# Kernel optimization log

Measured on AMD Instinct MI355X. Metric: run time of the kernel, lower is better.

The kernel has to match this reference:

```python
import jax, jax.numpy as jnp
import numpy as np

B, N = 16, 16384
K = 16        # num_keypoints
LATENT = 128
CAGE = 8
BN_EPS = 1e-5


def setup_inputs():
    key = jax.random.key(0)
    ks = jax.random.split(key, 40)
    def rn(i, shape, s=1.0):
        return jax.random.normal(ks[i], shape, dtype=jnp.float32) * s
    inp = {
        "source_points": rn(0, (B, N, 3)),
        "target_points": rn(1, (B, N, 3)),
        "enc_w1": rn(2, (64, 3), 0.3), "enc_b1": rn(3, (64,), 0.1),
        "bn1_gamma": 1.0 + rn(4, (64,), 0.1), "bn1_beta": rn(5, (64,), 0.1),
        "bn1_mean": rn(6, (64,), 0.1), "bn1_var": 0.5 + jax.random.uniform(ks[7], (64,), dtype=jnp.float32),
        "enc_w2": rn(8, (128, 64), 0.1), "enc_b2": rn(9, (128,), 0.1),
        "bn2_gamma": 1.0 + rn(10, (128,), 0.1), "bn2_beta": rn(11, (128,), 0.1),
        "bn2_mean": rn(12, (128,), 0.1), "bn2_var": 0.5 + jax.random.uniform(ks[13], (128,), dtype=jnp.float32),
        "enc_w3": rn(14, (LATENT, 128), 0.1), "enc_b3": rn(15, (LATENT,), 0.1),
        "bn3_gamma": 1.0 + rn(16, (LATENT,), 0.1), "bn3_beta": rn(17, (LATENT,), 0.1),
        "bn3_mean": rn(18, (LATENT,), 0.1), "bn3_var": 0.5 + jax.random.uniform(ks[19], (LATENT,), dtype=jnp.float32),
        "kp_w1": rn(20, (128, LATENT), 0.1), "kp_b1": rn(21, (128,), 0.1),
        "kp_w2": rn(22, (K * 3, 128), 0.1), "kp_b2": rn(23, (K * 3,), 0.1),
        "cg_w1": rn(24, (128, K * 3), 0.1), "cg_b1": rn(25, (128,), 0.1),
        "cg_w2": rn(26, (CAGE ** 3 * 3, 128), 0.05), "cg_b2": rn(27, (CAGE ** 3 * 3,), 0.01),
    }
    return inp


def _bn(x, g, b, m, v):
    # inference-mode BatchNorm1d over channel (last) dim
    return (x - m) * jax.lax.rsqrt(v + BN_EPS) * g + b


def _encode(pts, w1, b1, g1, be1, m1, v1, w2, b2, g2, be2, m2, v2, w3, b3, g3, be3, m3, v3):
    # pointwise 1x1 convs == per-point linear layers; pts: (B, N, 3)
    h = jax.nn.relu(_bn(jnp.einsum('bnc,oc->bno', pts, w1) + b1, g1, be1, m1, v1))
    h = jax.nn.relu(_bn(jnp.einsum('bnc,oc->bno', h, w2) + b2, g2, be2, m2, v2))
    h = jax.nn.relu(_bn(jnp.einsum('bnc,oc->bno', h, w3) + b3, g3, be3, m3, v3))
    return h.max(axis=1)  # global max-pool -> (B, LATENT)


def _fps_one(pts, kps):
    # pts: (N,3), kps: (K,3). Same math as the torch loop: iterative farthest-point
    # selection; recomputing cdist to selected[:i] each step == incremental min-dist.
    # squared distances preserve argmax/min of euclidean distances.
    d0 = jnp.sum((pts[:, None, :] - kps[None, :, :]) ** 2, -1).min(axis=1)
    sel0 = pts[jnp.argmax(d0)]
    mind = jnp.sum((pts - sel0) ** 2, -1)
    def step(mind, _):
        sel = pts[jnp.argmax(mind)]
        return jnp.minimum(mind, jnp.sum((pts - sel) ** 2, -1)), sel
    _, sels = jax.lax.scan(step, mind, None, length=K - 1)
    return jnp.concatenate([sel0[None], sels], axis=0)  # (K, 3)


def _fps(points, keypoints):
    return jax.vmap(_fps_one)(points, keypoints)


def _cage_deform(pts, disp):
    # pts: (B,N,3), disp: (B,C,C,C,3). Batched trilinear interpolation on the cage.
    C = CAGE
    lin = jnp.linspace(0.0, 1.0, C)
    grid = jnp.stack(jnp.meshgrid(lin, lin, lin, indexing='ij'), axis=-1)
    cage = grid[None] + disp
    cf = cage.reshape(cage.shape[0], C * C * C, 3)
    pmin = pts.min(axis=1, keepdims=True)
    pmax = pts.max(axis=1, keepdims=True)
    t = (pts - pmin) / (pmax - pmin + 1e-6) * (C - 1)
    idx = jnp.clip(t.astype(jnp.int32), 0, C - 2)   # trunc == floor (t >= 0)
    w = t - idx.astype(t.dtype)
    u, v, z = idx[..., 0], idx[..., 1], idx[..., 2]
    wx, wy, wz = w[..., 0:1], w[..., 1:2], w[..., 2:3]
    def corner(du, dv, dz):
        flat = (u + du) * C * C + (v + dv) * C + (z + dz)      # (B,N)
        flat = jnp.broadcast_to(flat[..., None], flat.shape + (3,))
        return jnp.take_along_axis(cf, flat, axis=1)            # (B,N,3)
    d = ((1 - wx) * (1 - wy) * (1 - wz) * corner(0, 0, 0)
         + wx * (1 - wy) * (1 - wz) * corner(1, 0, 0)
         + (1 - wx) * wy * (1 - wz) * corner(0, 1, 0)
         + wx * wy * (1 - wz) * corner(1, 1, 0)
         + (1 - wx) * (1 - wy) * wz * corner(0, 0, 1)
         + wx * (1 - wy) * wz * corner(1, 0, 1)
         + (1 - wx) * wy * wz * corner(0, 1, 1)
         + wx * wy * wz * corner(1, 1, 1))
    return pts + d


def reference(source_points, target_points, enc_w1, enc_b1, bn1_gamma, bn1_beta, bn1_mean, bn1_var, enc_w2, enc_b2, bn2_gamma, bn2_beta, bn2_mean, bn2_var, enc_w3, enc_b3, bn3_gamma, bn3_beta, bn3_mean, bn3_var, kp_w1, kp_b1, kp_w2, kp_b2, cg_w1, cg_b1, cg_w2, cg_b2):
    enc = lambda p: _encode(p, enc_w1, enc_b1, bn1_gamma, bn1_beta, bn1_mean, bn1_var,
                            enc_w2, enc_b2, bn2_gamma, bn2_beta, bn2_mean, bn2_var,
                            enc_w3, enc_b3, bn3_gamma, bn3_beta, bn3_mean, bn3_var)
    src_lat = enc(source_points)
    tgt_lat = enc(target_points)
    kp = lambda lat: (jax.nn.relu(lat @ kp_w1.T + kp_b1) @ kp_w2.T + kp_b2).reshape(-1, K, 3)
    src_kp = _fps(source_points, kp(src_lat))
    tgt_kp = _fps(target_points, kp(tgt_lat))
    diff = (tgt_kp - src_kp).reshape(-1, K * 3)
    disp = (jax.nn.relu(diff @ cg_w1.T + cg_b1) @ cg_w2.T + cg_b2).reshape(-1, CAGE, CAGE, CAGE, 3)
    deformed = _cage_deform(source_points, disp)
    return (deformed, src_kp, tgt_kp)
```

## Files before the change

kernel.cpp:

```cpp
#include <hip/hip_runtime.h>

#define B_ 16
#define N_ 16384
#define K_ 16

enum : int {
  WS_LAT  = 0,
  WS_SEL  = 5632,
  WS_PMIN = 7168,
  WS_PMAX = 7216,
  WS_CF   = 7264,
  WS_W1F  = 31840,
  WS_B1F  = 32032,
  WS_WB2H = 32096,
  WS_WB2L = 36192,
  WS_B2F  = 40288,
  WS_WB3H = 40416,
  WS_B3F  = 56800,
  WS_WB3L = 56928,
  WS_END  = 73312
};

enum : int { OUT_DEF=0, OUT_SRCKP=786432, OUT_TGTKP=787200 };

typedef _Float16 f16x8 __attribute__((ext_vector_type(8)));
typedef _Float16 f16x2 __attribute__((ext_vector_type(2)));
typedef float    f32x16 __attribute__((ext_vector_type(16)));

__device__ __forceinline__ float dist2rn(float px,float py,float pz,float sx,float sy,float sz){
  float dx=__fsub_rn(px,sx), dy=__fsub_rn(py,sy), dz=__fsub_rn(pz,sz);
  return __fadd_rn(__fadd_rn(__fmul_rn(dx,dx),__fmul_rn(dy,dy)),__fmul_rn(dz,dz));
}

struct EncW {
  const float *w1,*b1,*g1,*be1,*m1,*v1;
  const float *w2,*b2,*g2,*be2,*m2,*v2;
  const float *w3,*b3,*g3,*be3,*m3,*v3;
};

__device__ __forceinline__ float bn_scale(const float* g, const float* v, int ch){
  return g[ch] * (1.0f / sqrtf(v[ch] + 1e-5f));
}

__global__ void prep_kernel(EncW a, float* ws){
  const int stride = gridDim.x*blockDim.x;
  const int tid = blockIdx.x*blockDim.x + threadIdx.x;
  for (int i=tid;i<4096;i+=stride)
    ws[WS_LAT+i] = 0.0f;
  for (int i=tid;i<192;i+=stride){
    int o=i/3;
    ws[WS_W1F+i] = a.w1[i] * bn_scale(a.g1,a.v1,o);
  }
  for (int i=tid;i<64;i+=stride){
    float s = bn_scale(a.g1,a.v1,i);
    ws[WS_B1F+i] = (a.b1[i] - a.m1[i])*s + a.be1[i];
  }
  for (int i=tid;i<8192;i+=stride){
    int j = i & 7, frag = i >> 3;
    int l = frag & 63, wk = frag >> 6;
    int kt = wk & 3, wn = wk >> 2;
    int c = kt*16 + ((l>>5)<<3) + j;
    int o = wn*32 + (l&31);
    float v = a.w2[o*64+c] * bn_scale(a.g2,a.v2,o);
    _Float16 h = (_Float16)v;
    ((_Float16*)(ws+WS_WB2H))[i] = h;
    ((_Float16*)(ws+WS_WB2L))[i] = (_Float16)(v - (float)h);
  }
  for (int i=tid;i<128;i+=stride){
    float s = bn_scale(a.g2,a.v2,i);
    ws[WS_B2F+i] = (a.b2[i] - a.m2[i])*s + a.be2[i];
  }
  for (int i=tid;i<16384;i+=stride){
    int j = i & 7, frag = i >> 3;
    int l = frag & 63, wk = frag >> 6;
    int kt = wk & 7, wn = wk >> 3;
    int c = kt*16 + ((l>>5)<<3) + j;
    int o = wn*32 + (l&31);
    float v = a.w3[o*128+c] * bn_scale(a.g3,a.v3,o);
    _Float16 h = (_Float16)v;
    ((_Float16*)(ws+WS_WB3H))[i] = h;
    ((_Float16*)(ws+WS_WB3L))[i] = (_Float16)(v - (float)h);
  }
  for (int i=tid;i<128;i+=stride){
    float s = bn_scale(a.g3,a.v3,i);
    ws[WS_B3F+i] = (a.b3[i] - a.m3[i])*s + a.be3[i];
  }
}

__global__ __launch_bounds__(256, 5) void encode_kernel(const float* __restrict__ src,
                                                        const float* __restrict__ tgt,
                                                        const float* __restrict__ ws,
                                                        float* __restrict__ lat){
  const int cloud = blockIdx.y;
  const int tile  = blockIdx.x;
  const int t = threadIdx.x;
  const int lane = t & 63;
  const int wn = __builtin_amdgcn_readfirstlane(t >> 6);
  const int l31 = lane & 31;
  const int hb  = lane >> 5;
  const int swz = (l31 & 7) << 3;

  __shared__ alignas(16) _Float16 A[16384];

  const float* base = ((cloud < B_) ? (src + (size_t)cloud*N_*3)
                                    : (tgt + (size_t)(cloud-B_)*N_*3))
                      + (size_t)tile*64*3;

  f16x8 b2h[4], b2l[4];
  {
    const _Float16* wb2h = (const _Float16*)(ws + WS_WB2H);
    const _Float16* wb2l = (const _Float16*)(ws + WS_WB2L);
    #pragma unroll
    for (int kt=0; kt<4; kt++){
      const int fi = ((wn*4 + kt)*64 + lane)*8;
      b2h[kt] = *(const f16x8*)(wb2h + fi);
      b2l[kt] = *(const f16x8*)(wb2l + fi);
    }
  }

  {
    const int pt = t >> 2, q = t & 3;
    const float x = base[pt*3+0], y = base[pt*3+1], z = base[pt*3+2];
    const float* w1 = ws + WS_W1F;
    const float* b1 = ws + WS_B1F;
    const int swz1 = (pt & 7) << 3;
    _Float16* AH1 = A;
    _Float16* AL1 = A + 4096;
    #pragma unroll
    for (int cc = 0; cc < 16; cc += 2){
      const int o = q*16 + cc;
      float v0 = fmaf(w1[o*3+2], z, fmaf(w1[o*3+1], y, w1[o*3+0]*x)) + b1[o];
      float v1 = fmaf(w1[o*3+5], z, fmaf(w1[o*3+4], y, w1[o*3+3]*x)) + b1[o+1];
      v0 = fmaxf(v0, 0.0f); v1 = fmaxf(v1, 0.0f);
      f16x2 h, l;
      h[0] = (_Float16)v0;              h[1] = (_Float16)v1;
      l[0] = (_Float16)(v0 - (float)h[0]); l[1] = (_Float16)(v1 - (float)h[1]);
      const int idx = (pt*64 + o) ^ swz1;
      *(f16x2*)&AH1[idx] = h;
      *(f16x2*)&AL1[idx] = l;
    }
  }

  int koff[8];
  #pragma unroll
  for (int kt=0; kt<8; kt++) koff[kt] = (((kt*16) | (hb*8)) ^ swz) << 1;

  __syncthreads();

  f32x16 acc2[2];
  #pragma unroll
  for (int e=0;e<16;e++){ acc2[0][e]=0.0f; acc2[1][e]=0.0f; }
  {
    const char* pA2 = (const char*)A + l31*128;
    #pragma unroll
    for (int kt=0; kt<4; kt++){
      #pragma unroll
      for (int m=0;m<2;m++){
        const f16x8 ah = *(const f16x8*)(pA2 + m*4096 + koff[kt]);
        const f16x8 al = *(const f16x8*)(pA2 + m*4096 + koff[kt] + 8192);
        acc2[m] = __builtin_amdgcn_mfma_f32_32x32x16_f16(ah, b2h[kt], acc2[m], 0,0,0);
        acc2[m] = __builtin_amdgcn_mfma_f32_32x32x16_f16(ah, b2l[kt], acc2[m], 0,0,0);
        acc2[m] = __builtin_amdgcn_mfma_f32_32x32x16_f16(al, b2h[kt], acc2[m], 0,0,0);
      }
    }
  }
  __syncthreads();

  const int ch = wn*32 + l31;
  {
    const float b = ws[WS_B2F + ch];
    char* pWr[4];
    #pragma unroll
    for (int r4=0;r4<4;r4++)
      pWr[r4] = (char*)A + (r4 + 4*hb)*256 + ((ch ^ ((r4 + 4*hb) << 3)) << 1);
    #pragma unroll
    for (int r4=0;r4<4;r4++){
      #pragma unroll
      for (int rq=0;rq<4;rq++){
        const int reg = rq*4 + r4;
        #pragma unroll
        for (int m=0;m<2;m++){
          const float v = fmaxf(acc2[m][reg] + b, 0.0f);
          const _Float16 hi = (_Float16)v;
          const _Float16 lo = (_Float16)(v - (float)hi);
          char* pw = pWr[r4] + rq*2048 + m*8192;
          *(_Float16*)(pw) = hi;
          *(_Float16*)(pw + 16384) = lo;
        }
      }
    }
  }
  __syncthreads();

  f32x16 acc3[2];
  #pragma unroll
  for (int e=0;e<16;e++){ acc3[0][e]=0.0f; acc3[1][e]=0.0f; }
  {
    const _Float16* wb3h = (const _Float16*)(ws + WS_WB3H);
    const _Float16* wb3l = (const _Float16*)(ws + WS_WB3L);
    const char* pA3 = (const char*)A + l31*256;
    #pragma unroll
    for (int kt=0; kt<8; kt++){
      const int fi = ((wn*8 + kt)*64 + lane)*8;
      const f16x8 bh = *(const f16x8*)(wb3h + fi);
      const f16x8 bl = *(const f16x8*)(wb3l + fi);
      #pragma unroll
      for (int m=0;m<2;m++){
        const f16x8 ah = *(const f16x8*)(pA3 + m*8192 + koff[kt]);
        const f16x8 al = *(const f16x8*)(pA3 + m*8192 + koff[kt] + 16384);
        acc3[m] = __builtin_amdgcn_mfma_f32_32x32x16_f16(ah, bh, acc3[m], 0,0,0);
        acc3[m] = __builtin_amdgcn_mfma_f32_32x32x16_f16(ah, bl, acc3[m], 0,0,0);
        acc3[m] = __builtin_amdgcn_mfma_f32_32x32x16_f16(al, bh, acc3[m], 0,0,0);
      }
    }
  }

  {
    const float b = ws[WS_B3F + ch];
    float x = 0.0f;
    #pragma unroll
    for (int m=0;m<2;m++){
      #pragma unroll
      for (int r=0;r<16;r++)
        x = fmaxf(x, acc3[m][r] + b);
    }
    x = fmaxf(x, __shfl_xor(x, 32, 64));
    if (lane < 32)
      atomicMax((unsigned*)(lat + cloud*128 + ch), __float_as_uint(x));
  }
}

__device__ __forceinline__ void fps_round(int r, int t, int wv,
                                          float bv, int bi, float bx, float by, float bz,
                                          float (*cv)[16], int (*ci)[16],
                                          float (*cx)[16], float (*cy)[16], float (*cz)[16],
                                          float* ws, float* out, int cloud,
                                          float& s0, float& s1, float& s2){
  float v = bv; int i = bi;
  #pragma unroll
  for (int m=1;m<64;m<<=1){
    float v2=__shfl_xor(v,m,64); int i2=__shfl_xor(i,m,64);
    if (v2 > v || (v2 == v && i2 < i)){ v=v2; i=i2; }
  }
  const int p = r & 1;
  if ((i >> 4) == t){ cv[p][wv]=v; ci[p][wv]=i; cx[p][wv]=bx; cy[p][wv]=by; cz[p][wv]=bz; }
  __syncthreads();
  float wvv = cv[p][0]; int wi = ci[p][0]; int slot = 0;
  #pragma unroll
  for (int e=1;e<16;e++){
    float v2=cv[p][e]; int i2=ci[p][e];
    if (v2 > wvv || (v2 == wvv && i2 < wi)){ wvv=v2; wi=i2; slot=e; }
  }
  s0 = cx[p][slot]; s1 = cy[p][slot]; s2 = cz[p][slot];
  if (t == 0){
    float* sw = ws + WS_SEL + cloud*48 + r*3;
    sw[0]=s0; sw[1]=s1; sw[2]=s2;
    size_t o = (cloud<B_) ? (size_t)(OUT_SRCKP + cloud*48 + r*3)
                          : (size_t)(OUT_TGTKP + (cloud-B_)*48 + r*3);
    out[o]=s0; out[o+1]=s1; out[o+2]=s2;
  }
}

__global__ __launch_bounds__(1024, 4) void fps_kernel(const float* __restrict__ src,
                                                      const float* __restrict__ tgt,
                                                      const float* __restrict__ kw1,
                                                      const float* __restrict__ kb1,
                                                      const float* __restrict__ kw2,
                                                      const float* __restrict__ kb2,
                                                      float* ws, float* out){
  const int cloud = blockIdx.x; const int t = threadIdx.x;
  const int wv = t >> 6;
  const int lane = t & 63;
  const float* base = (cloud < B_) ? (src + (size_t)cloud*N_*3)
                                   : (tgt + (size_t)cloud*N_*3 - (size_t)B_*N_*3);
  __shared__ alignas(16) float kpl[48];
  __shared__ alignas(16) float h[128];
  __shared__ float cv[2][16]; __shared__ int ci[2][16];
  __shared__ float cx[2][16]; __shared__ float cy[2][16]; __shared__ float cz[2][16];
  __shared__ float red[96];

  float px[16], py[16], pz[16];
  {
    float4 raw[12];
    const float4* b4 = (const float4*)(base + (size_t)t*48);
    #pragma unroll
    for (int q=0;q<12;q++) raw[q] = b4[q];
    #pragma unroll
    for (int q=0;q<4;q++){
      float4 va=raw[q*3], vb=raw[q*3+1], vc=raw[q*3+2];
      px[q*4  ]=va.x; py[q*4  ]=va.y; pz[q*4  ]=va.z;
      px[q*4+1]=va.w; py[q*4+1]=vb.x; pz[q*4+1]=vb.y;
      px[q*4+2]=vb.z; py[q*4+2]=vb.w; pz[q*4+2]=vc.x;
      px[q*4+3]=vc.y; py[q*4+3]=vc.z; pz[q*4+3]=vc.w;
    }
  }
  #pragma unroll
  for (int k=0;k<16;k++){
    asm volatile("" : "+v"(px[k]), "+v"(py[k]), "+v"(pz[k]));
  }

  const float* lat = ws + WS_LAT + cloud*128;
  if (t < 128){
    float acc = kb1[t];
    const float4* w4 = (const float4*)(kw1 + t*128);
    const float4* l4 = (const float4*)lat;
    #pragma unroll 8
    for (int c4=0;c4<32;c4++){
      float4 wq=w4[c4], lq=l4[c4];
      acc = fmaf(lq.x, wq.x, acc);
      acc = fmaf(lq.y, wq.y, acc);
      acc = fmaf(lq.z, wq.z, acc);
      acc = fmaf(lq.w, wq.w, acc);
    }
    h[t] = fmaxf(acc, 0.0f);
  }
  __syncthreads();
  if (t < 48){
    float acc = kb2[t];
    const float4* w4 = (const float4*)(kw2 + t*128);
    #pragma unroll 8
    for (int c4=0;c4<32;c4++){
      float4 wq=w4[c4];
      float4 hq=*(const float4*)&h[c4*4];
      acc = fmaf(hq.x, wq.x, acc);
      acc = fmaf(hq.y, wq.y, acc);
      acc = fmaf(hq.z, wq.z, acc);
      acc = fmaf(hq.w, wq.w, acc);
    }
    kpl[t] = acc;
  }

  if (cloud < B_){
    float mn0=3.4e38f,mn1=3.4e38f,mn2=3.4e38f, mx0=-3.4e38f,mx1=-3.4e38f,mx2=-3.4e38f;
    #pragma unroll
    for (int k=0;k<16;k++){
      mn0=fminf(mn0,px[k]); mn1=fminf(mn1,py[k]); mn2=fminf(mn2,pz[k]);
      mx0=fmaxf(mx0,px[k]); mx1=fmaxf(mx1,py[k]); mx2=fmaxf(mx2,pz[k]);
    }
    #pragma unroll
    for (int m=1;m<64;m<<=1){
      mn0=fminf(mn0,__shfl_xor(mn0,m,64)); mx0=fmaxf(mx0,__shfl_xor(mx0,m,64));
      mn1=fminf(mn1,__shfl_xor(mn1,m,64)); mx1=fmaxf(mx1,__shfl_xor(mx1,m,64));
      mn2=fminf(mn2,__shfl_xor(mn2,m,64)); mx2=fmaxf(mx2,__shfl_xor(mx2,m,64));
    }
    if (lane==0){
      red[wv*6+0]=mn0; red[wv*6+1]=mn1; red[wv*6+2]=mn2;
      red[wv*6+3]=mx0; red[wv*6+4]=mx1; red[wv*6+5]=mx2;
    }
    __syncthreads();
    if (t < 6){
      float v = red[t];
      for (int e=1;e<16;e++){
        float v2 = red[e*6+t];
        v = (t<3) ? fminf(v,v2) : fmaxf(v,v2);
      }
      if (t<3) ws[WS_PMIN + cloud*3 + t] = v;
      else     ws[WS_PMAX + cloud*3 + (t-3)] = v;
    }
  }
  __syncthreads();

  float mind[16];
  #pragma unroll
  for (int k=0;k<16;k++) mind[k] = 3.4028235e38f;
  for (int j=0;j<K_;j++){
    const float sx=kpl[j*3], sy=kpl[j*3+1], sz=kpl[j*3+2];
    #pragma unroll
    for (int k=0;k<16;k++)
      mind[k] = fminf(mind[k], dist2rn(px[k],py[k],pz[k], sx,sy,sz));
  }

  float bv = -1.0f; int bi = 0; float bx=0.f, by=0.f, bz=0.f;
  #pragma unroll
  for (int k=0;k<16;k++){
    if (mind[k] > bv){ bv=mind[k]; bi=t*16+k; bx=px[k]; by=py[k]; bz=pz[k]; }
  }
  float s0, s1, s2;
  fps_round(0, t, wv, bv, bi, bx, by, bz, cv, ci, cx, cy, cz, ws, out, cloud, s0, s1, s2);

  bv = -1.0f; bi = 0;
  #pragma unroll
  for (int k=0;k<16;k++){
    float d = dist2rn(px[k],py[k],pz[k], s0,s1,s2);
    mind[k] = d;
    if (d > bv){ bv=d; bi=t*16+k; bx=px[k]; by=py[k]; bz=pz[k]; }
  }
  fps_round(1, t, wv, bv, bi, bx, by, bz, cv, ci, cx, cy, cz, ws, out, cloud, s0, s1, s2);

  for (int r=2; r<K_; ++r){
    bv = -1.0f; bi = 0;
    #pragma unroll
    for (int k=0;k<16;k++){
      float d = dist2rn(px[k],py[k],pz[k], s0,s1,s2);
      float m = fminf(mind[k], d);
      mind[k] = m;
      if (m > bv){ bv=m; bi=t*16+k; bx=px[k]; by=py[k]; bz=pz[k]; }
    }
    fps_round(r, t, wv, bv, bi, bx, by, bz, cv, ci, cx, cy, cz, ws, out, cloud, s0, s1, s2);
  }
}

__global__ __launch_bounds__(256) void deform_kernel(const float* __restrict__ src,
                                                     const float* __restrict__ cw1,
                                                     const float* __restrict__ cb1,
                                                     const float* __restrict__ cw2,
                                                     const float* __restrict__ cb2,
                                                     const float* __restrict__ ws,
                                                     float* __restrict__ out){
  const int b = blockIdx.y;
  const int t = threadIdx.x;
  __shared__ float cf[1536];
  __shared__ alignas(16) float diff[48];
  __shared__ alignas(16) float hh[128];

  if (t<48) diff[t] = __fsub_rn(ws[WS_SEL + (B_+b)*48 + t], ws[WS_SEL + b*48 + t]);
  __syncthreads();
  if (t<128){
    const float4* w4 = (const float4*)(cw1 + t*48);
    float acc = cb1[t];
    #pragma unroll
    for (int j4=0;j4<12;j4++){
      float4 wq=w4[j4];
      float4 dq=*(const float4*)&diff[j4*4];
      acc = fmaf(dq.x, wq.x, acc);
      acc = fmaf(dq.y, wq.y, acc);
      acc = fmaf(dq.z, wq.z, acc);
      acc = fmaf(dq.w, wq.w, acc);
    }
    hh[t] = fmaxf(acc, 0.0f);
  }
  __syncthreads();
  for (int o = t; o < 1536; o += 256){
    const float4* w4 = (const float4*)(cw2 + o*128);
    float acc = cb2[o];
    #pragma unroll 8
    for (int c4=0;c4<32;c4++){
      float4 wq=w4[c4];
      float4 hq=*(const float4*)&hh[c4*4];
      acc = fmaf(hq.x, wq.x, acc);
      acc = fmaf(hq.y, wq.y, acc);
      acc = fmaf(hq.z, wq.z, acc);
      acc = fmaf(hq.w, wq.w, acc);
    }
    int flat = o/3, coord = o - flat*3;
    int u = flat>>6, v=(flat>>3)&7, z=flat&7;
    int g = (coord==0)?u:((coord==1)?v:z);
    float gv = (g==7)?1.0f:(float)g*(1.0f/7.0f);
    cf[o] = gv + acc;
  }
  __syncthreads();

  const float mn0 = ws[WS_PMIN+b*3+0], mn1 = ws[WS_PMIN+b*3+1], mn2 = ws[WS_PMIN+b*3+2];
  const float mx0 = ws[WS_PMAX+b*3+0], mx1 = ws[WS_PMAX+b*3+1], mx2 = ws[WS_PMAX+b*3+2];

  #pragma unroll
  for (int k=0;k<4;k++){
    const int n = blockIdx.x*1024 + k*256 + t;
    const float* p = src + ((size_t)b*N_ + n)*3;
    float pt[3]; int id[3]; float w[3];
    #pragma unroll
    for (int c=0;c<3;c++){
      float pv = p[c];
      float mnv = (c==0)?mn0:((c==1)?mn1:mn2);
      float mxv = (c==0)?mx0:((c==1)?mx1:mx2);
      float denom = __fadd_rn(__fsub_rn(mxv, mnv), 1e-6f);
      float tc = __fmul_rn(__fdiv_rn(__fsub_rn(pv, mnv), denom), 7.0f);
      int ic = (int)tc; ic = min(max(ic,0),6);
      pt[c]=pv; id[c]=ic; w[c]=__fsub_rn(tc, (float)ic);
    }
    const int flat = (id[0]<<6) + (id[1]<<3) + id[2];
    const float* c000 = cf + flat*3;
    const float wx=w[0], wy=w[1], wz=w[2];
    const float ux=__fsub_rn(1.0f,wx), uy=__fsub_rn(1.0f,wy), uz=__fsub_rn(1.0f,wz);
    const float w000=__fmul_rn(__fmul_rn(ux,uy),uz);
    const float w100=__fmul_rn(__fmul_rn(wx,uy),uz);
    const float w010=__fmul_rn(__fmul_rn(ux,wy),uz);
    const float w110=__fmul_rn(__fmul_rn(wx,wy),uz);
    const float w001=__fmul_rn(__fmul_rn(ux,uy),wz);
    const float w101=__fmul_rn(__fmul_rn(wx,uy),wz);
    const float w011=__fmul_rn(__fmul_rn(ux,wy),wz);
    const float w111=__fmul_rn(__fmul_rn(wx,wy),wz);
    #pragma unroll
    for (int c=0;c<3;c++){
      float d = __fmul_rn(w000, c000[c]);
      d = __fadd_rn(d, __fmul_rn(w100, c000[192+c]));
      d = __fadd_rn(d, __fmul_rn(w010, c000[24+c]));
      d = __fadd_rn(d, __fmul_rn(w110, c000[216+c]));
      d = __fadd_rn(d, __fmul_rn(w001, c000[3+c]));
      d = __fadd_rn(d, __fmul_rn(w101, c000[195+c]));
      d = __fadd_rn(d, __fmul_rn(w011, c000[27+c]));
      d = __fadd_rn(d, __fmul_rn(w111, c000[219+c]));
      out[((size_t)b*N_+n)*3 + c] = __fadd_rn(pt[c], d);
    }
  }
}

extern "C" void kernel_launch(void* const* d_in, const int* in_sizes, int n_in,
                              void* d_out, int out_size, void* d_ws, size_t ws_size,
                              hipStream_t stream){
  const float* src = (const float*)d_in[0];
  const float* tgt = (const float*)d_in[1];
  float* ws = (float*)d_ws;
  float* out = (float*)d_out;

  EncW ew;
  ew.w1 =(const float*)d_in[2];  ew.b1 =(const float*)d_in[3];
  ew.g1 =(const float*)d_in[4];  ew.be1=(const float*)d_in[5];
  ew.m1 =(const float*)d_in[6];  ew.v1 =(const float*)d_in[7];
  ew.w2 =(const float*)d_in[8];  ew.b2 =(const float*)d_in[9];
  ew.g2 =(const float*)d_in[10]; ew.be2=(const float*)d_in[11];
  ew.m2 =(const float*)d_in[12]; ew.v2 =(const float*)d_in[13];
  ew.w3 =(const float*)d_in[14]; ew.b3 =(const float*)d_in[15];
  ew.g3 =(const float*)d_in[16]; ew.be3=(const float*)d_in[17];
  ew.m3 =(const float*)d_in[18]; ew.v3 =(const float*)d_in[19];

  prep_kernel<<<128, 256, 0, stream>>>(ew, ws);
  encode_kernel<<<dim3(256,32), 256, 0, stream>>>(src, tgt, ws, ws + WS_LAT);
  fps_kernel<<<32, 1024, 0, stream>>>(src, tgt,
      (const float*)d_in[20], (const float*)d_in[21],
      (const float*)d_in[22], (const float*)d_in[23], ws, out);
  deform_kernel<<<dim3(16,16), 256, 0, stream>>>(src,
      (const float*)d_in[24], (const float*)d_in[25],
      (const float*)d_in[26], (const float*)d_in[27], ws, out);
}
```

Before: 295.0 us.

## Process two point tiles per encode block with interleaved software-pipelined stages

Each encode block now handles two 64-point tiles using two LDS buffers, interleaving layer-1 compute of tile B with layer-2 MFMAs of tile A, and so on, so ALU/LDS work overlaps matrix work and the barrier count per tile drops. The grid is halved and launch bounds drop from 5 to 2 waves-per-EU hints, doubling LDS per block. This trades occupancy and register pressure for intra-block overlap, and the same weight fragments are loaded once per two tiles.

```diff
diff --git a/kernel.cpp b/kernel.cpp
--- a/kernel.cpp
+++ b/kernel.cpp
@@ -87,24 +87,141 @@
   }
 }
 
-__global__ __launch_bounds__(256, 5) void encode_kernel(const float* __restrict__ src,
+
+__device__ __forceinline__ void enc_layer1(const float* __restrict__ base,
+                                           _Float16* __restrict__ Abuf,
+                                           const float* __restrict__ ws, int t){
+  const int pt = t >> 2, q = t & 3;
+  const float x = base[pt*3+0], y = base[pt*3+1], z = base[pt*3+2];
+  const float* w1 = ws + WS_W1F;
+  const float* b1 = ws + WS_B1F;
+  const int swz1 = (pt & 7) << 3;
+  _Float16* AH1 = Abuf;
+  _Float16* AL1 = Abuf + 4096;
+  #pragma unroll
+  for (int cc = 0; cc < 16; cc += 2){
+    const int o = q*16 + cc;
+    float v0 = fmaf(w1[o*3+2], z, fmaf(w1[o*3+1], y, w1[o*3+0]*x)) + b1[o];
+    float v1 = fmaf(w1[o*3+5], z, fmaf(w1[o*3+4], y, w1[o*3+3]*x)) + b1[o+1];
+    v0 = fmaxf(v0, 0.0f); v1 = fmaxf(v1, 0.0f);
+    f16x2 h, l;
+    h[0] = (_Float16)v0;              h[1] = (_Float16)v1;
+    l[0] = (_Float16)(v0 - (float)h[0]); l[1] = (_Float16)(v1 - (float)h[1]);
+    const int idx = (pt*64 + o) ^ swz1;
+    *(f16x2*)&AH1[idx] = h;
+    *(f16x2*)&AL1[idx] = l;
+  }
+}
+
+__device__ __forceinline__ void enc_layer2(const _Float16* __restrict__ Abuf,
+                                           const f16x8 b2h[4], const f16x8 b2l[4],
+                                           const int koff[8], int l31,
+                                           f32x16 acc2[2]){
+  #pragma unroll
+  for (int e=0;e<16;e++){ acc2[0][e]=0.0f; acc2[1][e]=0.0f; }
+  const char* pA2 = (const char*)Abuf + l31*128;
+  #pragma unroll
+  for (int kt=0; kt<4; kt++){
+    #pragma unroll
+    for (int m=0;m<2;m++){
+      const f16x8 ah = *(const f16x8*)(pA2 + m*4096 + koff[kt]);
+      const f16x8 al = *(const f16x8*)(pA2 + m*4096 + koff[kt] + 8192);
+      acc2[m] = __builtin_amdgcn_mfma_f32_32x32x16_f16(ah, b2h[kt], acc2[m], 0,0,0);
+      acc2[m] = __builtin_amdgcn_mfma_f32_32x32x16_f16(ah, b2l[kt], acc2[m], 0,0,0);
+      acc2[m] = __builtin_amdgcn_mfma_f32_32x32x16_f16(al, b2h[kt], acc2[m], 0,0,0);
+    }
+  }
+}
+
+__device__ __forceinline__ void enc_h2store(_Float16* __restrict__ Abuf,
+                                            const f32x16 acc2[2],
+                                            const float* __restrict__ ws,
+                                            int ch, int hb){
+  const float b = ws[WS_B2F + ch];
+  char* pWr[4];
+  #pragma unroll
+  for (int r4=0;r4<4;r4++)
+    pWr[r4] = (char*)Abuf + (r4 + 4*hb)*256 + ((ch ^ ((r4 + 4*hb) << 3)) << 1);
+  #pragma unroll
+  for (int r4=0;r4<4;r4++){
+    #pragma unroll
+    for (int rq=0;rq<4;rq++){
+      const int reg = rq*4 + r4;
+      #pragma unroll
+      for (int m=0;m<2;m++){
+        const float v = fmaxf(acc2[m][reg] + b, 0.0f);
+        const _Float16 hi = (_Float16)v;
+        const _Float16 lo = (_Float16)(v - (float)hi);
+        char* pw = pWr[r4] + rq*2048 + m*8192;
+        *(_Float16*)(pw) = hi;
+        *(_Float16*)(pw + 16384) = lo;
+      }
+    }
+  }
+}
+
+__device__ __forceinline__ void enc_layer3(const _Float16* __restrict__ Abuf,
+                                           const float* __restrict__ ws,
+                                           const int koff[8], int l31, int wn, int lane,
+                                           f32x16 acc3[2]){
+  #pragma unroll
+  for (int e=0;e<16;e++){ acc3[0][e]=0.0f; acc3[1][e]=0.0f; }
+  const _Float16* wb3h = (const _Float16*)(ws + WS_WB3H);
+  const _Float16* wb3l = (const _Float16*)(ws + WS_WB3L);
+  const char* pA3 = (const char*)Abuf + l31*256;
+  #pragma unroll
+  for (int kt=0; kt<8; kt++){
+    const int fi = ((wn*8 + kt)*64 + lane)*8;
+    const f16x8 bh = *(const f16x8*)(wb3h + fi);
+    const f16x8 bl = *(const f16x8*)(wb3l + fi);
+    #pragma unroll
+    for (int m=0;m<2;m++){
+      const f16x8 ah = *(const f16x8*)(pA3 + m*8192 + koff[kt]);
+      const f16x8 al = *(const f16x8*)(pA3 + m*8192 + koff[kt] + 16384);
+      acc3[m] = __builtin_amdgcn_mfma_f32_32x32x16_f16(ah, bh, acc3[m], 0,0,0);
+      acc3[m] = __builtin_amdgcn_mfma_f32_32x32x16_f16(ah, bl, acc3[m], 0,0,0);
+      acc3[m] = __builtin_amdgcn_mfma_f32_32x32x16_f16(al, bh, acc3[m], 0,0,0);
+    }
+  }
+}
+
+__device__ __forceinline__ void enc_epilogue(const f32x16 acc3[2],
+                                             const float* __restrict__ ws,
+                                             float* __restrict__ lat,
+                                             int ch, int lane, int cloud){
+  const float b = ws[WS_B3F + ch];
+  float x = 0.0f;
+  #pragma unroll
+  for (int m=0;m<2;m++){
+    #pragma unroll
+    for (int r=0;r<16;r++)
+      x = fmaxf(x, acc3[m][r] + b);
+  }
+  x = fmaxf(x, __shfl_xor(x, 32, 64));
+  if (lane < 32)
+    atomicMax((unsigned*)(lat + cloud*128 + ch), __float_as_uint(x));
+}
+
+__global__ __launch_bounds__(256, 2) void encode_kernel(const float* __restrict__ src,
                                                         const float* __restrict__ tgt,
                                                         const float* __restrict__ ws,
                                                         float* __restrict__ lat){
   const int cloud = blockIdx.y;
-  const int tile  = blockIdx.x;
   const int t = threadIdx.x;
   const int lane = t & 63;
   const int wn = __builtin_amdgcn_readfirstlane(t >> 6);
   const int l31 = lane & 31;
   const int hb  = lane >> 5;
   const int swz = (l31 & 7) << 3;
-
-  __shared__ alignas(16) _Float16 A[16384];
-
-  const float* base = ((cloud < B_) ? (src + (size_t)cloud*N_*3)
-                                    : (tgt + (size_t)(cloud-B_)*N_*3))
-                      + (size_t)tile*64*3;
+  const int ch = wn*32 + l31;
+
+  __shared__ alignas(16) _Float16 A0[16384];
+  __shared__ alignas(16) _Float16 A1[16384];
+
+  const float* cbase = (cloud < B_) ? (src + (size_t)cloud*N_*3)
+                                    : (tgt + (size_t)(cloud-B_)*N_*3);
+  const float* base0 = cbase + (size_t)(blockIdx.x*2    )*64*3;
+  const float* base1 = cbase + (size_t)(blockIdx.x*2 + 1)*64*3;
 
   f16x8 b2h[4], b2l[4];
   {
@@ -118,116 +235,32 @@
     }
   }
 
-  {
-    const int pt = t >> 2, q = t & 3;
-    const float x = base[pt*3+0], y = base[pt*3+1], z = base[pt*3+2];
-    const float* w1 = ws + WS_W1F;
-    const float* b1 = ws + WS_B1F;
-    const int swz1 = (pt & 7) << 3;
-    _Float16* AH1 = A;
-    _Float16* AL1 = A + 4096;
-    #pragma unroll
-    for (int cc = 0; cc < 16; cc += 2){
-      const int o = q*16 + cc;
-      float v0 = fmaf(w1[o*3+2], z, fmaf(w1[o*3+1], y, w1[o*3+0]*x)) + b1[o];
-      float v1 = fmaf(w1[o*3+5], z, fmaf(w1[o*3+4], y, w1[o*3+3]*x)) + b1[o+1];
-      v0 = fmaxf(v0, 0.0f); v1 = fmaxf(v1, 0.0f);
-      f16x2 h, l;
-      h[0] = (_Float16)v0;              h[1] = (_Float16)v1;
-      l[0] = (_Float16)(v0 - (float)h[0]); l[1] = (_Float16)(v1 - (float)h[1]);
-      const int idx = (pt*64 + o) ^ swz1;
-      *(f16x2*)&AH1[idx] = h;
-      *(f16x2*)&AL1[idx] = l;
-    }
-  }
-
   int koff[8];
   #pragma unroll
   for (int kt=0; kt<8; kt++) koff[kt] = (((kt*16) | (hb*8)) ^ swz) << 1;
 
-  __syncthreads();
-
-  f32x16 acc2[2];
-  #pragma unroll
-  for (int e=0;e<16;e++){ acc2[0][e]=0.0f; acc2[1][e]=0.0f; }
-  {
-    const char* pA2 = (const char*)A + l31*128;
-    #pragma unroll
-    for (int kt=0; kt<4; kt++){
-      #pragma unroll
-      for (int m=0;m<2;m++){
-        const f16x8 ah = *(const f16x8*)(pA2 + m*4096 + koff[kt]);
-        const f16x8 al = *(const f16x8*)(pA2 + m*4096 + koff[kt] + 8192);
-        acc2[m] = __builtin_amdgcn_mfma_f32_32x32x16_f16(ah, b2h[kt], acc2[m], 0,0,0);
-        acc2[m] = __builtin_amdgcn_mfma_f32_32x32x16_f16(ah, b2l[kt], acc2[m], 0,0,0);
-        acc2[m] = __builtin_amdgcn_mfma_f32_32x32x16_f16(al, b2h[kt], acc2[m], 0,0,0);
-      }
-    }
-  }
-  __syncthreads();
-
-  const int ch = wn*32 + l31;
-  {
-    const float b = ws[WS_B2F + ch];
-    char* pWr[4];
-    #pragma unroll
-    for (int r4=0;r4<4;r4++)
-      pWr[r4] = (char*)A + (r4 + 4*hb)*256 + ((ch ^ ((r4 + 4*hb) << 3)) << 1);
-    #pragma unroll
-    for (int r4=0;r4<4;r4++){
-      #pragma unroll
-      for (int rq=0;rq<4;rq++){
-        const int reg = rq*4 + r4;
-        #pragma unroll
-        for (int m=0;m<2;m++){
-          const float v = fmaxf(acc2[m][reg] + b, 0.0f);
-          const _Float16 hi = (_Float16)v;
-          const _Float16 lo = (_Float16)(v - (float)hi);
-          char* pw = pWr[r4] + rq*2048 + m*8192;
-          *(_Float16*)(pw) = hi;
-          *(_Float16*)(pw + 16384) = lo;
-        }
-      }
-    }
-  }
-  __syncthreads();
-
-  f32x16 acc3[2];
-  #pragma unroll
-  for (int e=0;e<16;e++){ acc3[0][e]=0.0f; acc3[1][e]=0.0f; }
-  {
-    const _Float16* wb3h = (const _Float16*)(ws + WS_WB3H);
-    const _Float16* wb3l = (const _Float16*)(ws + WS_WB3L);
-    const char* pA3 = (const char*)A + l31*256;
-    #pragma unroll
-    for (int kt=0; kt<8; kt++){
-      const int fi = ((wn*8 + kt)*64 + lane)*8;
-      const f16x8 bh = *(const f16x8*)(wb3h + fi);
-      const f16x8 bl = *(const f16x8*)(wb3l + fi);
-      #pragma unroll
-      for (int m=0;m<2;m++){
-        const f16x8 ah = *(const f16x8*)(pA3 + m*8192 + koff[kt]);
-        const f16x8 al = *(const f16x8*)(pA3 + m*8192 + koff[kt] + 16384);
-        acc3[m] = __builtin_amdgcn_mfma_f32_32x32x16_f16(ah, bh, acc3[m], 0,0,0);
-        acc3[m] = __builtin_amdgcn_mfma_f32_32x32x16_f16(ah, bl, acc3[m], 0,0,0);
-        acc3[m] = __builtin_amdgcn_mfma_f32_32x32x16_f16(al, bh, acc3[m], 0,0,0);
-      }
-    }
-  }
-
-  {
-    const float b = ws[WS_B3F + ch];
-    float x = 0.0f;
-    #pragma unroll
-    for (int m=0;m<2;m++){
-      #pragma unroll
-      for (int r=0;r<16;r++)
-        x = fmaxf(x, acc3[m][r] + b);
-    }
-    x = fmaxf(x, __shfl_xor(x, 32, 64));
-    if (lane < 32)
-      atomicMax((unsigned*)(lat + cloud*128 + ch), __float_as_uint(x));
-  }
+  enc_layer1(base0, A0, ws, t);
+  __syncthreads();
+
+  f32x16 acc2a[2];
+  enc_layer2(A0, b2h, b2l, koff, l31, acc2a);
+  enc_layer1(base1, A1, ws, t);
+  __syncthreads();
+
+  enc_h2store(A0, acc2a, ws, ch, hb);
+  f32x16 acc2b[2];
+  enc_layer2(A1, b2h, b2l, koff, l31, acc2b);
+  __syncthreads();
+
+  f32x16 acc3a[2];
+  enc_layer3(A0, ws, koff, l31, wn, lane, acc3a);
+  enc_h2store(A1, acc2b, ws, ch, hb);
+  __syncthreads();
+
+  f32x16 acc3b[2];
+  enc_layer3(A1, ws, koff, l31, wn, lane, acc3b);
+  enc_epilogue(acc3a, ws, lat, ch, lane, cloud);
+  enc_epilogue(acc3b, ws, lat, ch, lane, cloud);
 }
 
 __device__ __forceinline__ void fps_round(int r, int t, int wv,
@@ -515,7 +548,7 @@
   ew.m3 =(const float*)d_in[18]; ew.v3 =(const float*)d_in[19];
 
   prep_kernel<<<128, 256, 0, stream>>>(ew, ws);
-  encode_kernel<<<dim3(256,32), 256, 0, stream>>>(src, tgt, ws, ws + WS_LAT);
+  encode_kernel<<<dim3(128,32), 256, 0, stream>>>(src, tgt, ws, ws + WS_LAT);
   fps_kernel<<<32, 1024, 0, stream>>>(src, tgt,
       (const float*)d_in[20], (const float*)d_in[21],
       (const float*)d_in[22], (const float*)d_in[23], ws, out);
```

After: 335.1 us. 1.14x slower.
